# Performance work log

Hardware: AMD Instinct MI355X
Metric: run time of the kernel (lower is better)

Reference implementation:

```python
import jax, jax.numpy as jnp
import numpy as np

NUM_HEADS = 16
NUM_KV_HEADS = 4
HEAD_DIM = 128
ROPE_BASE = 10000.0


def _apply_rope(x):
    # x: [B, H, S, D], interleaved RoPE: x1 = x[..., ::2], x2 = x[..., 1::2]
    B, H, S, D = x.shape
    inv_freq = 1.0 / (ROPE_BASE ** (jnp.arange(0, D, 2, dtype=jnp.float32) / D))  # [D/2]
    t = jnp.arange(S, dtype=jnp.float32)
    freqs = t[:, None] * inv_freq[None, :]          # [S, D/2]
    cos = jnp.cos(freqs)[None, None]                # [1,1,S,D/2]
    sin = jnp.sin(freqs)[None, None]
    xr = x.reshape(B, H, S, D // 2, 2)
    x1, x2 = xr[..., 0], xr[..., 1]
    r1 = x1 * cos - x2 * sin
    r2 = x1 * sin + x2 * cos
    return jnp.stack([r1, r2], axis=-1).reshape(B, H, S, D)


def setup_inputs() -> dict:
    key = jax.random.key(0)
    ks = jax.random.split(key, 5)
    H = NUM_HEADS * HEAD_DIM          # 2048
    KV = NUM_KV_HEADS * HEAD_DIM      # 512
    std = 0.02
    return {
        "hidden_states": jax.random.normal(ks[0], (1, 4096, H), dtype=jnp.float32),
        "wq": jax.random.normal(ks[1], (H, H), dtype=jnp.float32) * std,
        "wk": jax.random.normal(ks[2], (H, KV), dtype=jnp.float32) * std,
        "wv": jax.random.normal(ks[3], (H, KV), dtype=jnp.float32) * std,
        "wo": jax.random.normal(ks[4], (H, H), dtype=jnp.float32) * std,
    }


def reference(hidden_states, wq, wk, wv, wo):
    B, S, H = hidden_states.shape
    nh, nkv, hd = NUM_HEADS, NUM_KV_HEADS, HEAD_DIM
    scale = 1.0 / np.sqrt(hd)

    q = (hidden_states @ wq).reshape(B, S, nh, hd).transpose(0, 2, 1, 3)   # [B,nh,S,hd]
    k = (hidden_states @ wk).reshape(B, S, nkv, hd).transpose(0, 2, 1, 3)  # [B,nkv,S,hd]
    v = (hidden_states @ wv).reshape(B, S, nkv, hd).transpose(0, 2, 1, 3)

    q = _apply_rope(q)
    k = _apply_rope(k)

    rep = nh // nkv
    k = jnp.repeat(k, rep, axis=1)  # GQA head repetition -> [B,nh,S,hd]
    v = jnp.repeat(v, rep, axis=1)

    scores = jnp.einsum("bhqd,bhkd->bhqk", q, k) * scale
    causal = jnp.tril(jnp.ones((S, S), dtype=bool))
    scores = jnp.where(causal[None, None], scores, jnp.float32(-1e30))
    probs = jax.nn.softmax(scores, axis=-1)
    attn = jnp.einsum("bhqk,bhkd->bhqd", probs, v)      # [B,nh,S,hd]
    attn = attn.transpose(0, 2, 1, 3).reshape(B, S, H)
    return attn @ wo
```

## Files before the change

### kernel.cpp

```cpp
#include <hip/hip_runtime.h>

typedef unsigned short u16;
typedef unsigned int u32;
typedef __bf16 bf16x8 __attribute__((ext_vector_type(8)));
typedef float f32x4 __attribute__((ext_vector_type(4)));
typedef float f32x16 __attribute__((ext_vector_type(16)));
typedef int v2i __attribute__((ext_vector_type(2)));

#define S_LEN 4096
#define HDIM 2048
#define KVDIM 512
#define N_HEADS 16
#define HEAD_D 128

__device__ __forceinline__ u16 f2bf(float f) {
  u32 u = __float_as_uint(f);
  u32 r = (u + 0x7FFFu + ((u >> 16) & 1u)) >> 16;
  return (u16)r;
}
__device__ __forceinline__ float bf2f(u16 h) {
  return __uint_as_float(((u32)h) << 16);
}
__device__ __forceinline__ float exp2_fast(float x) {
  float r;
  asm("v_exp_f32 %0, %1" : "=v"(r) : "v"(x));
  return r;
}
__device__ __forceinline__ u32 cvt_pk_bf16(float lo, float hi) {
  u32 r;
  asm("v_cvt_pk_bf16_f32 %0, %1, %2" : "=v"(r) : "v"(lo), "v"(hi));
  return r;
}
__device__ __forceinline__ void gload16(const u16* g, const u16* l) {
  __builtin_amdgcn_global_load_lds(
      (const __attribute__((address_space(1))) void*)g,
      (__attribute__((address_space(3))) void*)l, 16, 0, 0);
}

__global__ void k_prep(const float* __restrict__ in, u16* __restrict__ out,
                       float* __restrict__ cosT, float* __restrict__ sinT) {
  int b = blockIdx.x;
  int tid = threadIdx.x;
  if (b < 4096) {
    int i = b * 256 + tid;
    const float4* p = reinterpret_cast<const float4*>(in) + (size_t)i * 2;
    float4 a = p[0], c = p[1];
    u32 o0 = (u32)f2bf(a.x) | ((u32)f2bf(a.y) << 16);
    u32 o1 = (u32)f2bf(a.z) | ((u32)f2bf(a.w) << 16);
    u32 o2 = (u32)f2bf(c.x) | ((u32)f2bf(c.y) << 16);
    u32 o3 = (u32)f2bf(c.z) | ((u32)f2bf(c.w) << 16);
    reinterpret_cast<uint4*>(out)[i] = make_uint4(o0, o1, o2, o3);
  } else {
    int i = (b - 4096) * 256 + tid;
    int pos = i >> 6, f = i & 63;
    float inv = expf(-0.1439115683121279f * (float)f);
    float ang = (float)pos * inv;
    float s, c;
    sincosf(ang, &s, &c);
    cosT[i] = c;
    sinT[i] = s;
  }
}

__global__ void k_transpose_all(const float* __restrict__ wq, const float* __restrict__ wk,
                                const float* __restrict__ wv, const float* __restrict__ wo,
                                u16* __restrict__ WqT, u16* __restrict__ WkT,
                                u16* __restrict__ WvT, u16* __restrict__ WoT) {
  __shared__ float t[32][33];
  int b = blockIdx.x;
  const float* W;
  u16* Wt;
  int Kd, Nd, bx, by;
  if (b < 4096) {
    W = wq; Wt = WqT; Kd = HDIM; Nd = HDIM; bx = b & 63; by = b >> 6;
  } else if (b < 5120) {
    int r = b - 4096; W = wk; Wt = WkT; Kd = HDIM; Nd = KVDIM; bx = r & 15; by = r >> 4;
  } else if (b < 6144) {
    int r = b - 5120; W = wv; Wt = WvT; Kd = HDIM; Nd = KVDIM; bx = r & 15; by = r >> 4;
  } else {
    int r = b - 6144; W = wo; Wt = WoT; Kd = HDIM; Nd = HDIM; bx = r & 63; by = r >> 6;
  }
  int tx = threadIdx.x & 31, ty = threadIdx.x >> 5;
  int n = bx * 32 + tx;
  for (int j = ty; j < 32; j += 8)
    t[j][tx] = W[(size_t)(by * 32 + j) * Nd + n];
  __syncthreads();
  int k = by * 32 + tx;
  for (int j = ty; j < 32; j += 8)
    Wt[(size_t)(bx * 32 + j) * Kd + k] = f2bf(t[tx][j]);
}

__global__ void k_rope_all(u16* __restrict__ Qb, u16* __restrict__ Kb,
                           const float* __restrict__ cosT, const float* __restrict__ sinT) {
  int b = blockIdx.x;
  u16* X;
  int width, i;
  if (b < 4096) { X = Qb; width = HDIM; i = b * 256 + threadIdx.x; }
  else { X = Kb; width = KVDIM; i = (b - 4096) * 256 + threadIdx.x; }
  size_t idx = (size_t)i * 8;
  int row = (int)(idx / width);
  int col = (int)(idx - (size_t)row * width);
  int fi = (col & 127) >> 1;
  float4 c4 = *reinterpret_cast<const float4*>(&cosT[(row << 6) + fi]);
  float4 s4 = *reinterpret_cast<const float4*>(&sinT[(row << 6) + fi]);
  uint4 v = *reinterpret_cast<const uint4*>(&X[idx]);
  float cc[4] = {c4.x, c4.y, c4.z, c4.w};
  float ss[4] = {s4.x, s4.y, s4.z, s4.w};
  u32 w_[4] = {v.x, v.y, v.z, v.w};
  u32 r_[4];
#pragma unroll
  for (int p = 0; p < 4; ++p) {
    float x1 = bf2f((u16)(w_[p] & 0xffff));
    float x2 = bf2f((u16)(w_[p] >> 16));
    float r1 = x1 * cc[p] - x2 * ss[p];
    float r2 = x1 * ss[p] + x2 * cc[p];
    r_[p] = (u32)f2bf(r1) | ((u32)f2bf(r2) << 16);
  }
  *reinterpret_cast<uint4*>(&X[idx]) = make_uint4(r_[0], r_[1], r_[2], r_[3]);
}

__global__ __launch_bounds__(256) void k_gemm_qkv(
    const u16* __restrict__ A, const u16* __restrict__ WqT, const u16* __restrict__ WkT,
    const u16* __restrict__ WvT, u16* __restrict__ Qb, u16* __restrict__ Kb,
    u16* __restrict__ VTb) {
  const int Kd = HDIM, M = S_LEN;
  __shared__ __align__(16) u16 As[128 * 32];
  __shared__ __align__(16) u16 Bs[128 * 32];
  const int p = blockIdx.x;
  const int bmg = p & 7, r = p >> 3;
  const int bm = (bmg * 4 + (r & 3)) * 128;
  const int by = r >> 2;
  const u16* Bt;
  int bn, N, mode;
  if (by < 16) { Bt = WqT; bn = by * 128; N = HDIM; mode = 0; }
  else if (by < 20) { Bt = WkT; bn = (by - 16) * 128; N = KVDIM; mode = 1; }
  else { Bt = WvT; bn = (by - 20) * 128; N = KVDIM; mode = 2; }
  const int tid = threadIdx.x;
  const int lane = tid & 63;
  const int wid = tid >> 6;
  const int wr = (wid >> 1) * 64, wc = (wid & 1) * 64;
  const int lr = lane & 15, lhi = lane >> 4;
  const int srow = lane >> 2;
  const int skc = (lane & 3) * 8;
  f32x4 acc[4][4] = {};
  for (int k0 = 0; k0 < Kd; k0 += 32) {
#pragma unroll
    for (int it = 0; it < 2; ++it) {
      int rowbase = (it * 4 + wid) * 16;
      gload16(&A[(size_t)(bm + rowbase + srow) * Kd + k0 + skc], &As[rowbase * 32]);
      gload16(&Bt[(size_t)(bn + rowbase + srow) * Kd + k0 + skc], &Bs[rowbase * 32]);
    }
    __syncthreads();
    bf16x8 af[4], bfr[4];
#pragma unroll
    for (int m = 0; m < 4; ++m)
      af[m] = *reinterpret_cast<const bf16x8*>(&As[(wr + m * 16 + lr) * 32 + lhi * 8]);
#pragma unroll
    for (int n = 0; n < 4; ++n)
      bfr[n] = *reinterpret_cast<const bf16x8*>(&Bs[(wc + n * 16 + lr) * 32 + lhi * 8]);
#pragma unroll
    for (int m = 0; m < 4; ++m)
#pragma unroll
      for (int n = 0; n < 4; ++n)
        acc[m][n] = __builtin_amdgcn_mfma_f32_16x16x32_bf16(af[m], bfr[n], acc[m][n], 0, 0, 0);
    __syncthreads();
  }
#pragma unroll
  for (int m = 0; m < 4; ++m) {
    int grow0 = bm + wr + m * 16 + lhi * 4;
#pragma unroll
    for (int n = 0; n < 4; ++n) {
      int gcol = bn + wc + n * 16 + lr;
      if (mode == 2) {
        ushort4 pk;
        pk.x = f2bf(acc[m][n][0]);
        pk.y = f2bf(acc[m][n][1]);
        pk.z = f2bf(acc[m][n][2]);
        pk.w = f2bf(acc[m][n][3]);
        *reinterpret_cast<ushort4*>(&VTb[(size_t)gcol * M + grow0]) = pk;
      } else {
        u16* outp = (mode == 0) ? Qb : Kb;
#pragma unroll
        for (int r2 = 0; r2 < 4; ++r2)
          outp[(size_t)(grow0 + r2) * N + gcol] = f2bf(acc[m][n][r2]);
      }
    }
  }
}

__global__ __launch_bounds__(256) void k_gemm_bt(
    const u16* __restrict__ A, const u16* __restrict__ Bt, float* __restrict__ Cout,
    int M, int N, int Kd) {
  __shared__ __align__(16) u16 As[128 * 32];
  __shared__ __align__(16) u16 Bs[128 * 32];
  const int p = blockIdx.x;
  const int bmg = p & 7, r = p >> 3;
  const int bm = (bmg * 4 + (r & 3)) * 128;
  const int bn = (r >> 2) * 128;
  const int tid = threadIdx.x;
  const int lane = tid & 63;
  const int wid = tid >> 6;
  const int wr = (wid >> 1) * 64, wc = (wid & 1) * 64;
  const int lr = lane & 15, lhi = lane >> 4;
  const int srow = lane >> 2;
  const int skc = (lane & 3) * 8;
  f32x4 acc[4][4] = {};
  for (int k0 = 0; k0 < Kd; k0 += 32) {
#pragma unroll
    for (int it = 0; it < 2; ++it) {
      int rowbase = (it * 4 + wid) * 16;
      gload16(&A[(size_t)(bm + rowbase + srow) * Kd + k0 + skc], &As[rowbase * 32]);
      gload16(&Bt[(size_t)(bn + rowbase + srow) * Kd + k0 + skc], &Bs[rowbase * 32]);
    }
    __syncthreads();
    bf16x8 af[4], bfr[4];
#pragma unroll
    for (int m = 0; m < 4; ++m)
      af[m] = *reinterpret_cast<const bf16x8*>(&As[(wr + m * 16 + lr) * 32 + lhi * 8]);
#pragma unroll
    for (int n = 0; n < 4; ++n)
      bfr[n] = *reinterpret_cast<const bf16x8*>(&Bs[(wc + n * 16 + lr) * 32 + lhi * 8]);
#pragma unroll
    for (int m = 0; m < 4; ++m)
#pragma unroll
      for (int n = 0; n < 4; ++n)
        acc[m][n] = __builtin_amdgcn_mfma_f32_16x16x32_bf16(af[m], bfr[n], acc[m][n], 0, 0, 0);
    __syncthreads();
  }
#pragma unroll
  for (int m = 0; m < 4; ++m) {
    int grow0 = bm + wr + m * 16 + lhi * 4;
#pragma unroll
    for (int n = 0; n < 4; ++n) {
      int gcol = bn + wc + n * 16 + lr;
#pragma unroll
      for (int r2 = 0; r2 < 4; ++r2)
        Cout[(size_t)(grow0 + r2) * N + gcol] = acc[m][n][r2];
    }
  }
}

__global__ __launch_bounds__(256, 2) void k_attn(
    const u16* __restrict__ Q, const u16* __restrict__ K, const u16* __restrict__ VT,
    u16* __restrict__ O) {
  __shared__ __align__(16) u16 Ks[64 * 128];
  __shared__ __align__(16) u16 Vs[128 * 64];
  int i = blockIdx.x;
  int qt, h;
  if (i < 256) { qt = 16 + (i & 15); h = i >> 4; }
  else { int jj = i - 256; qt = 15 - (jj & 15); h = jj >> 4; }
  const int kvh = h >> 2;
  const int tid = threadIdx.x, lane = tid & 63, wid = tid >> 6;
  const int l31 = lane & 31, hi = lane >> 5;
  const int qw = qt * 128 + wid * 32;
  const int qglob = qw + l31;
  const float CE = 0.12751743f;
  const float THR = 62.74f;

  const u16* qptr = &Q[(size_t)qglob * HDIM + h * HEAD_D];
  bf16x8 qf[8];
#pragma unroll
  for (int ks = 0; ks < 8; ++ks)
    qf[ks] = *reinterpret_cast<const bf16x8*>(&qptr[ks * 16 + hi * 8]);

  f32x16 o_[4] = {};
  float m_ = -3e38f, l_ = 0.f;
  char* KsB = (char*)Ks;
  char* VsB = (char*)Vs;

  const int nst = 2 * qt + 2;
  for (int j = 0; j < nst; ++j) {
    const int kb = j << 6;
    __syncthreads();
#pragma unroll
    for (int it = 0; it < 4; ++it) {
      int s = it * 256 + tid;
      int kv = s >> 4, c16 = s & 15;
      int db = kv * 256 + c16 * 16;
      db ^= ((db >> 8) & 7) << 4;
      *reinterpret_cast<uint4*>(KsB + db) = *reinterpret_cast<const uint4*>(
          &K[(size_t)(kb + kv) * KVDIM + kvh * HEAD_D + c16 * 8]);
    }
#pragma unroll
    for (int it = 0; it < 4; ++it) {
      int s = it * 256 + tid;
      int d = s >> 3, k16 = s & 7;
      int db = d * 128 + k16 * 16;
      db ^= ((db >> 7) & 7) << 4;
      *reinterpret_cast<uint4*>(VsB + db) = *reinterpret_cast<const uint4*>(
          &VT[(size_t)(kvh * HEAD_D + d) * S_LEN + kb + k16 * 8]);
    }
    __syncthreads();

    if (kb <= qw + 31) {
      f32x16 s0 = {}, s1 = {};
#pragma unroll
      for (int ks = 0; ks < 8; ++ks) {
        int db0 = l31 * 256 + ks * 32 + hi * 16;
        db0 ^= ((db0 >> 8) & 7) << 4;
        int db1 = (32 + l31) * 256 + ks * 32 + hi * 16;
        db1 ^= ((db1 >> 8) & 7) << 4;
        bf16x8 k0 = *reinterpret_cast<const bf16x8*>(KsB + db0);
        bf16x8 k1 = *reinterpret_cast<const bf16x8*>(KsB + db1);
        s0 = __builtin_amdgcn_mfma_f32_32x32x16_bf16(k0, qf[ks], s0, 0, 0, 0);
        s1 = __builtin_amdgcn_mfma_f32_32x32x16_bf16(k1, qf[ks], s1, 0, 0, 0);
      }
      if (kb + 63 > qw) {
#pragma unroll
        for (int r = 0; r < 16; ++r) {
          int kvr = kb + (r & 3) + 8 * (r >> 2) + 4 * hi;
          if (kvr > qglob) s0[r] = -1e30f;
          if (kvr + 32 > qglob) s1[r] = -1e30f;
        }
      }
      float pm = fmaxf(s0[0], s1[0]);
#pragma unroll
      for (int r = 1; r < 16; ++r) pm = fmaxf(pm, fmaxf(s0[r], s1[r]));
      pm = fmaxf(pm, __shfl_xor(pm, 32));
      if (!__all(pm <= m_ + THR)) {
        float mnew = fmaxf(m_, pm);
        float fac = exp2_fast((m_ - mnew) * CE);
        m_ = mnew;
        l_ *= fac;
#pragma unroll
        for (int dt = 0; dt < 4; ++dt)
#pragma unroll
          for (int r = 0; r < 16; ++r) o_[dt][r] *= fac;
      }
      const float mc = m_ * CE;
      float rs = 0.f;
#pragma unroll
      for (int r = 0; r < 16; ++r) {
        s0[r] = exp2_fast(__builtin_fmaf(s0[r], CE, -mc));
        s1[r] = exp2_fast(__builtin_fmaf(s1[r], CE, -mc));
        rs += s0[r] + s1[r];
      }
      rs += __shfl_xor(rs, 32);
      l_ += rs;
#pragma unroll
      for (int kvt = 0; kvt < 2; ++kvt) {
        u32 xw[8], yw[8];
#pragma unroll
        for (int g = 0; g < 8; ++g) {
          float plo = kvt ? s1[2 * g] : s0[2 * g];
          float phi = kvt ? s1[2 * g + 1] : s0[2 * g + 1];
          u32 pw = cvt_pk_bf16(plo, phi);
          v2i sw = __builtin_amdgcn_permlane32_swap((int)pw, (int)pw, false, false);
          xw[g] = (u32)sw[0];
          yw[g] = (u32)sw[1];
        }
#pragma unroll
        for (int ksl = 0; ksl < 2; ++ksl) {
          int b = ksl * 4;
          u32 f0 = hi ? xw[b + 2] : xw[b + 0];
          u32 f1 = hi ? xw[b + 3] : xw[b + 1];
          u32 f2 = hi ? yw[b + 2] : yw[b + 0];
          u32 f3 = hi ? yw[b + 3] : yw[b + 1];
          uint4 fr = make_uint4(f0, f1, f2, f3);
          bf16x8 pf = *reinterpret_cast<bf16x8*>(&fr);
          const int kvstep = kvt * 2 + ksl;
#pragma unroll
          for (int dt = 0; dt < 4; ++dt) {
            int db = (dt * 32 + l31) * 128 + kvstep * 32 + hi * 16;
            db ^= ((db >> 7) & 7) << 4;
            bf16x8 vf = *reinterpret_cast<const bf16x8*>(VsB + db);
            o_[dt] = __builtin_amdgcn_mfma_f32_32x32x16_bf16(vf, pf, o_[dt], 0, 0, 0);
          }
        }
      }
    }
  }
  const float inv_l = 1.0f / l_;
  u16* optr = &O[(size_t)qglob * HDIM + h * HEAD_D];
#pragma unroll
  for (int dt = 0; dt < 4; ++dt)
#pragma unroll
    for (int g = 0; g < 4; ++g) {
      ushort4 pk;
      pk.x = f2bf(o_[dt][4 * g + 0] * inv_l);
      pk.y = f2bf(o_[dt][4 * g + 1] * inv_l);
      pk.z = f2bf(o_[dt][4 * g + 2] * inv_l);
      pk.w = f2bf(o_[dt][4 * g + 3] * inv_l);
      *reinterpret_cast<ushort4*>(&optr[dt * 32 + g * 8 + hi * 4]) = pk;
    }
}

extern "C" void kernel_launch(void* const* d_in, const int* in_sizes, int n_in,
                              void* d_out, int out_size, void* d_ws, size_t ws_size,
                              hipStream_t stream) {
  const float* hs = (const float*)d_in[0];
  const float* wq = (const float*)d_in[1];
  const float* wk = (const float*)d_in[2];
  const float* wv = (const float*)d_in[3];
  const float* wo = (const float*)d_in[4];

  char* ws = (char*)d_ws;
  size_t off = 0;
  auto alloc = [&](size_t bytes) {
    void* p = ws + off;
    off += (bytes + 255) & ~(size_t)255;
    return p;
  };
  u16* Xb = (u16*)alloc((size_t)S_LEN * HDIM * 2);
  u16* WqT = (u16*)alloc((size_t)HDIM * HDIM * 2);
  u16* WkT = (u16*)alloc((size_t)KVDIM * HDIM * 2);
  u16* WvT = (u16*)alloc((size_t)KVDIM * HDIM * 2);
  u16* WoT = (u16*)alloc((size_t)HDIM * HDIM * 2);
  u16* Qb = (u16*)alloc((size_t)S_LEN * HDIM * 2);
  u16* Kb = (u16*)alloc((size_t)S_LEN * KVDIM * 2);
  u16* VTb = (u16*)alloc((size_t)KVDIM * S_LEN * 2);
  u16* Ab = (u16*)alloc((size_t)S_LEN * HDIM * 2);
  float* cosT = (float*)alloc((size_t)S_LEN * 64 * 4);
  float* sinT = (float*)alloc((size_t)S_LEN * 64 * 4);
  if (off > ws_size) return;

  k_prep<<<dim3(5120), dim3(256), 0, stream>>>(hs, Xb, cosT, sinT);
  k_transpose_all<<<dim3(10240), dim3(256), 0, stream>>>(wq, wk, wv, wo, WqT, WkT, WvT, WoT);
  k_gemm_qkv<<<dim3(768), dim3(256), 0, stream>>>(Xb, WqT, WkT, WvT, Qb, Kb, VTb);
  k_rope_all<<<dim3(5120), dim3(256), 0, stream>>>(Qb, Kb, cosT, sinT);
  k_attn<<<dim3(512), dim3(256), 0, stream>>>(Qb, Kb, VTb, Ab);
  k_gemm_bt<<<dim3(512), dim3(256), 0, stream>>>(Ab, WoT, (float*)d_out, S_LEN, HDIM, HDIM);
}
```

Measured before the change: 285.6 us.

## Split causal attention KV range into two halves with a combine kernel

Each attention block now handles only half of its query tile's key/value range, so the grid doubles to 1024 blocks. Each block writes a normalized partial output plus its row max and sum, and a new combine kernel merges the two partials with log-sum-exp weights. The launch bound is raised to 4 blocks per CU so all blocks can be resident at once. The cost is an extra kernel pass over the partial outputs and a tighter register budget that could cause spills. Scratch space reuses buffers that are dead by this stage.

```diff
diff --git a/kernel.cpp b/kernel.cpp
--- a/kernel.cpp
+++ b/kernel.cpp
@@ -240,15 +240,17 @@
   }
 }
 
-__global__ __launch_bounds__(256, 2) void k_attn(
+__global__ __launch_bounds__(256, 4) void k_attn(
     const u16* __restrict__ Q, const u16* __restrict__ K, const u16* __restrict__ VT,
-    u16* __restrict__ O) {
+    u16* __restrict__ PO0, u16* __restrict__ PO1, float2* __restrict__ ML) {
   __shared__ __align__(16) u16 Ks[64 * 128];
   __shared__ __align__(16) u16 Vs[128 * 64];
   int i = blockIdx.x;
+  const int kvhalf = i >> 9;
+  int jj = i & 511;
   int qt, h;
-  if (i < 256) { qt = 16 + (i & 15); h = i >> 4; }
-  else { int jj = i - 256; qt = 15 - (jj & 15); h = jj >> 4; }
+  if (jj < 256) { qt = 16 + (jj & 15); h = jj >> 4; }
+  else { int j2 = jj - 256; qt = 15 - (j2 & 15); h = j2 >> 4; }
   const int kvh = h >> 2;
   const int tid = threadIdx.x, lane = tid & 63, wid = tid >> 6;
   const int l31 = lane & 31, hi = lane >> 5;
@@ -268,8 +270,9 @@
   char* KsB = (char*)Ks;
   char* VsB = (char*)Vs;
 
-  const int nst = 2 * qt + 2;
-  for (int j = 0; j < nst; ++j) {
+  const int j0 = kvhalf * (qt + 1);
+  const int j1 = j0 + qt + 1;
+  for (int j = j0; j < j1; ++j) {
     const int kb = j << 6;
     __syncthreads();
 #pragma unroll
@@ -370,8 +373,9 @@
       }
     }
   }
-  const float inv_l = 1.0f / l_;
-  u16* optr = &O[(size_t)qglob * HDIM + h * HEAD_D];
+  const float inv_l = (l_ > 0.f) ? (1.0f / l_) : 0.f;
+  u16* PO = kvhalf ? PO1 : PO0;
+  u16* optr = &PO[(size_t)qglob * HDIM + h * HEAD_D];
 #pragma unroll
   for (int dt = 0; dt < 4; ++dt)
 #pragma unroll
@@ -383,6 +387,38 @@
       pk.w = f2bf(o_[dt][4 * g + 3] * inv_l);
       *reinterpret_cast<ushort4*>(&optr[dt * 32 + g * 8 + hi * 4]) = pk;
     }
+  if (hi == 0)
+    ML[(size_t)kvhalf * N_HEADS * S_LEN + (size_t)h * S_LEN + qglob] =
+        make_float2(m_, l_);
+}
+
+__global__ void k_combine(const u16* __restrict__ PO0, const u16* __restrict__ PO1,
+                          const float2* __restrict__ ML, u16* __restrict__ Out) {
+  int i = blockIdx.x * 256 + threadIdx.x;
+  int d8 = (i & 15) * 8;
+  int qh = i >> 4;
+  int h = qh & 15, q = qh >> 4;
+  const float CE = 0.12751743f;
+  float2 ml1 = ML[(size_t)h * S_LEN + q];
+  float2 ml2 = ML[(size_t)N_HEADS * S_LEN + (size_t)h * S_LEN + q];
+  float m = fmaxf(ml1.x, ml2.x);
+  float w1 = ml1.y * exp2_fast((ml1.x - m) * CE);
+  float w2 = ml2.y * exp2_fast((ml2.x - m) * CE);
+  float inv = 1.0f / (w1 + w2);
+  w1 *= inv;
+  w2 *= inv;
+  size_t base = (size_t)q * HDIM + h * HEAD_D + d8;
+  uint4 a = *reinterpret_cast<const uint4*>(&PO0[base]);
+  uint4 b = *reinterpret_cast<const uint4*>(&PO1[base]);
+  u32 aw[4] = {a.x, a.y, a.z, a.w}, bw[4] = {b.x, b.y, b.z, b.w};
+  u32 ow[4];
+#pragma unroll
+  for (int p = 0; p < 4; ++p) {
+    float lo = w1 * bf2f((u16)(aw[p] & 0xffff)) + w2 * bf2f((u16)(bw[p] & 0xffff));
+    float hi2 = w1 * bf2f((u16)(aw[p] >> 16)) + w2 * bf2f((u16)(bw[p] >> 16));
+    ow[p] = (u32)f2bf(lo) | ((u32)f2bf(hi2) << 16);
+  }
+  *reinterpret_cast<uint4*>(&Out[base]) = make_uint4(ow[0], ow[1], ow[2], ow[3]);
 }
 
 extern "C" void kernel_launch(void* const* d_in, const int* in_sizes, int n_in,
@@ -414,10 +450,15 @@
   float* sinT = (float*)alloc((size_t)S_LEN * 64 * 4);
   if (off > ws_size) return;
 
+  u16* PO0 = Ab;
+  u16* PO1 = Xb;
+  float2* ML = (float2*)WqT;
+
   k_prep<<<dim3(5120), dim3(256), 0, stream>>>(hs, Xb, cosT, sinT);
   k_transpose_all<<<dim3(10240), dim3(256), 0, stream>>>(wq, wk, wv, wo, WqT, WkT, WvT, WoT);
   k_gemm_qkv<<<dim3(768), dim3(256), 0, stream>>>(Xb, WqT, WkT, WvT, Qb, Kb, VTb);
   k_rope_all<<<dim3(5120), dim3(256), 0, stream>>>(Qb, Kb, cosT, sinT);
-  k_attn<<<dim3(512), dim3(256), 0, stream>>>(Qb, Kb, VTb, Ab);
+  k_attn<<<dim3(1024), dim3(256), 0, stream>>>(Qb, Kb, VTb, PO0, PO1, ML);
+  k_combine<<<dim3(4096), dim3(256), 0, stream>>>(PO0, PO1, ML, Ab);
   k_gemm_bt<<<dim3(512), dim3(256), 0, stream>>>(Ab, WoT, (float*)d_out, S_LEN, HDIM, HDIM);
 }
```

New measurement: 630.4 us. 2.21x slower.
